# Kernel optimization log

Hardware: AMD Instinct MI355X
Metric: run time of the kernel (lower is better)

Reference implementation:

```python
import jax, jax.numpy as jnp
import numpy as np

N = 500_000      # total points
B = 64           # graphs in batch
D_IN = 64        # input feature dim (conv.in_tensor_reps.dim)
D_HID = 128      # EdgeConv MLP hidden
D_OUT = 128      # EdgeConv MLP out


def setup_inputs() -> dict:
    key = jax.random.key(0)
    k = jax.random.split(key, 8)
    x = jax.random.normal(k[0], (N, D_IN), jnp.float32)
    pos = jax.random.normal(k[1], (N, 3), jnp.float32)
    batch = jnp.sort(jax.random.randint(k[2], (N,), 0, B, dtype=jnp.int32))
    lframes = jax.random.normal(k[3], (N, 3, 3), jnp.float32)
    fan1 = 2 * D_IN + 3
    W1 = jax.random.normal(k[4], (fan1, D_HID), jnp.float32) / np.sqrt(fan1)
    b1 = jnp.zeros((D_HID,), jnp.float32)
    W2 = jax.random.normal(k[5], (D_HID, D_OUT), jnp.float32) / np.sqrt(D_HID)
    b2 = jnp.zeros((D_OUT,), jnp.float32)
    return {"x": x, "pos": pos, "batch": batch, "lframes": lframes,
            "W1": W1, "b1": b1, "W2": W2, "b2": b2}


def reference(x, pos, batch, lframes, W1, b1, W2, b2):
    n = pos.shape[0]
    # scatter-mean: center of mass per graph
    counts = jax.ops.segment_sum(jnp.ones((n,), pos.dtype), batch, num_segments=B)
    coms = jax.ops.segment_sum(pos, batch, num_segments=B) / jnp.maximum(counts, 1.0)[:, None]
    # distance of each point to its graph's COM
    dist = jnp.linalg.norm(pos - coms[batch], axis=-1)
    # scatter-min argmin per graph (first occurrence, like torch_scatter.scatter_min)
    min_d = jax.ops.segment_min(dist, batch, num_segments=B)
    node_ids = jnp.arange(n, dtype=jnp.int32)
    cand = jnp.where(dist <= min_d[batch], node_ids, n)
    idx = jnp.minimum(jax.ops.segment_min(cand, batch, num_segments=B), n - 1)  # [B]
    # gathers for the destination (center) nodes
    x_dst = x[idx]          # [B, D_IN]
    pos_dst = pos[idx]      # [B, 3]
    lframes_dst = lframes[idx]  # [B, 3, 3]
    # EdgeConv over edge_index = [arange(N) -> batch]:
    # message_e = MLP([x_dst_i, x_src_j - x_dst_i, pos_j - pos_i]), max-aggregated per graph
    xd = x_dst[batch]                      # [N, D_IN]
    feat = jnp.concatenate([xd, x - xd, pos - pos_dst[batch]], axis=-1)  # [N, 2*D_IN+3]
    h = jax.nn.relu(feat @ W1 + b1)        # [N, D_HID]
    msg = h @ W2 + b2                      # [N, D_OUT]
    out = jax.ops.segment_max(msg, batch, num_segments=B)  # [B, D_OUT]
    return out, pos_dst, batch[idx], lframes_dst
```

## Files before the change

### kernel.cpp

```cpp
#include <hip/hip_runtime.h>
#include <hip/hip_bf16.h>

#define NPTS 500000
#define NGR  64
#define TR   128
#define NT2  ((NPTS + TR - 1) / TR)
#define CHUNK 4
#define NBLK ((NT2 + CHUNK - 1) / CHUNK)

typedef __bf16 bf16x8 __attribute__((ext_vector_type(8)));
typedef float f32x4 __attribute__((ext_vector_type(4)));
typedef unsigned int u32x4 __attribute__((ext_vector_type(4)));

#define OFF_OUTACC 6144
#define OFF_CBIAS  38912
#define OFF_W1PT   71680
#define OFF_W1AT   73728
#define OFF_W2T    90112

__device__ __forceinline__ unsigned mapf(float f) {
    union { float f; unsigned u; } v; v.f = f;
    return ((int)v.u >= 0) ? (v.u | 0x80000000u) : ~v.u;
}

#define GLOAD_LDS16(g, l) __builtin_amdgcn_global_load_lds(                 \
    (__attribute__((address_space(1))) void*)(g),                           \
    (__attribute__((address_space(3))) void*)(l), 16, 0, 0)

__global__ __launch_bounds__(1024) void k_pre(
                      const float* __restrict__ pos,
                      const int* __restrict__ batch,
                      const float* __restrict__ x,
                      const float* __restrict__ W1,
                      const float* __restrict__ b1,
                      const float* __restrict__ W2,
                      const float* __restrict__ lfr,
                      unsigned short* __restrict__ W1aT,
                      unsigned short* __restrict__ W2T,
                      float* __restrict__ W1pT,
                      unsigned* __restrict__ outacc,
                      float* __restrict__ cbias,
                      float* __restrict__ outf) {
    __shared__ double sd[16][3];
    __shared__ unsigned long long sk[16];
    __shared__ double scom[3];
    __shared__ int sid;
    __shared__ float sposd[3];
    __shared__ float sp[4][128];
    __shared__ int sse[2];

    int g = blockIdx.x, t = threadIdx.x;
    int lane = t & 63, wv = t >> 6;

    {
        int i = g * 1024 + t;
        if (i < 8192) {
            outacc[i] = 0u;
            int n = i >> 6, k = i & 63;
            unsigned short v = (unsigned short)(__builtin_bit_cast(unsigned, (float)(__bf16)W1[(64 + k) * 128 + n]) >> 16);
            W1aT[i ^ ((n & 7) << 3)] = v;
        } else if (i < 8192 + 16384) {
            int j = i - 8192; int n = j >> 7, k = j & 127;
            unsigned short v = (unsigned short)(__builtin_bit_cast(unsigned, (float)(__bf16)W2[k * 128 + n]) >> 16);
            W2T[j ^ ((n & 7) << 3)] = v;
        } else if (i < 8192 + 16384 + 512) {
            int j = i - 24576; int n = j >> 2, q = j & 3;
            W1pT[j] = (q < 3) ? W1[(128 + q) * 128 + n] : 0.f;
        }
    }

    if (t < 2) {
        int target = g + t;
        int lo = 0, hi = NPTS;
        while (lo < hi) {
            int mid = (lo + hi) >> 1;
            if (batch[mid] < target) lo = mid + 1; else hi = mid;
        }
        sse[t] = lo;
    }
    __syncthreads();
    int s = sse[0], e = sse[1];

    double sx = 0.0, sy = 0.0, sz = 0.0;
    for (int i = s + t; i < e; i += 1024) {
        sx += (double)pos[i * 3 + 0];
        sy += (double)pos[i * 3 + 1];
        sz += (double)pos[i * 3 + 2];
    }
    #pragma unroll
    for (int m = 1; m < 64; m <<= 1) {
        sx += __shfl_xor(sx, m);
        sy += __shfl_xor(sy, m);
        sz += __shfl_xor(sz, m);
    }
    if (lane == 0) { sd[wv][0] = sx; sd[wv][1] = sy; sd[wv][2] = sz; }
    __syncthreads();
    if (t == 0) {
        double ax = 0.0, ay = 0.0, az = 0.0;
        for (int q = 0; q < 16; ++q) { ax += sd[q][0]; ay += sd[q][1]; az += sd[q][2]; }
        double cnt = (double)(e - s);
        double rc = 1.0 / (cnt > 1.0 ? cnt : 1.0);
        scom[0] = ax * rc; scom[1] = ay * rc; scom[2] = az * rc;
    }
    __syncthreads();
    double cx = scom[0], cy = scom[1], cz = scom[2];

    unsigned long long key = ~0ULL;
    for (int i = s + t; i < e; i += 1024) {
        double dx = (double)pos[i * 3 + 0] - cx;
        double dy = (double)pos[i * 3 + 1] - cy;
        double dz = (double)pos[i * 3 + 2] - cz;
        double d2 = __builtin_fma(dx, dx, __builtin_fma(dy, dy, dz * dz));
        unsigned long long b = __builtin_bit_cast(unsigned long long, d2);
        unsigned long long k2 = (b & ~0xFFFFFULL) | (unsigned long long)i;
        key = k2 < key ? k2 : key;
    }
    #pragma unroll
    for (int m = 1; m < 64; m <<= 1) {
        unsigned long long o = __shfl_xor(key, m);
        key = o < key ? o : key;
    }
    if (lane == 0) sk[wv] = key;
    __syncthreads();
    if (t == 0) {
        unsigned long long k = sk[0];
        for (int q = 1; q < 16; ++q) if (sk[q] < k) k = sk[q];
        int id = (int)(k & 0xFFFFFULL);
        if (id > NPTS - 1) id = NPTS - 1;
        sid = id;
    }
    __syncthreads();
    int id = sid;

    if (t < 3) {
        float p = pos[id * 3 + t];
        sposd[t] = p;
        outf[8192 + g * 3 + t] = p;
    }
    if (t == 4) outf[8192 + 192 + g] = (float)batch[id];
    if (t < 9) outf[8192 + 256 + g * 9 + t] = lfr[id * 9 + t];

    if (t < 512) {
        int c = t & 127, p = t >> 7;
        float part = 0.f;
        #pragma unroll
        for (int kq = 0; kq < 16; ++kq) {
            int k = p * 16 + kq;
            float xd = x[id * 64 + k];
            part += xd * (W1[k * 128 + c] - W1[(64 + k) * 128 + c]);
        }
        sp[p][c] = part;
    }
    __syncthreads();
    if (t < 128) {
        int c = t;
        float sv = b1[c] + sp[0][c] + sp[1][c] + sp[2][c] + sp[3][c];
        sv -= sposd[0] * W1[128 * 128 + c] + sposd[1] * W1[129 * 128 + c] + sposd[2] * W1[130 * 128 + c];
        cbias[g * 128 + c] = sv;
    }
}

__global__ __launch_bounds__(512, 2) void k_main(
    const float* __restrict__ x,
    const float* __restrict__ pos,
    const int* __restrict__ batch,
    const unsigned short* __restrict__ W1aT,
    const unsigned short* __restrict__ W2T,
    const float* __restrict__ W1pT,
    const float* __restrict__ cbias,
    unsigned* __restrict__ outacc)
{
    __shared__ alignas(16) unsigned char smem[81920];

    const int tid  = threadIdx.x;
    const int w    = tid >> 6;
    const int lane = tid & 63;
    const int quad = lane >> 4;
    const int mr   = lane & 15;

    #pragma unroll
    for (int i = 0; i < 6; ++i)
        GLOAD_LDS16((const char*)W1aT + (i * 512 + tid) * 16,
                    (char*)smem + (i * 512 + tid) * 16);

    bf16x8 bfrE[8];
    #pragma unroll
    for (int t8 = 0; t8 < 8; ++t8) {
        f32x4 wp = *(const f32x4*)(W1pT + (t8 * 16 + mr) * 4);
        bf16x8 e = (bf16x8){0, 0, 0, 0, 0, 0, 0, 0};
        if (quad == 0) { e[0] = (__bf16)wp[0]; e[1] = (__bf16)wp[1]; e[2] = (__bf16)wp[2]; }
        bfrE[t8] = e;
    }

    __syncthreads();

    const unsigned short* sW1 = (const unsigned short*)smem;
    const unsigned short* sW2 = (const unsigned short*)(smem + 16384);
    __bf16* hsb = (__bf16*)(smem + 49152) + w * 2048;
    const unsigned short* hss = (const unsigned short*)hsb;

    const int tb = blockIdx.x * CHUNK;
    int te = tb + CHUNK; if (te > NT2) te = NT2;

    f32x4 av0, av1, av2, av3;
    float pv0, pv1, pv2;
    {
        int gr = tb * TR + 16 * w + mr; if (gr > NPTS - 1) gr = NPTS - 1;
        const float* xp = x + (size_t)gr * 64 + quad * 8;
        av0 = *(const f32x4*)(xp);
        av1 = *(const f32x4*)(xp + 4);
        av2 = *(const f32x4*)(xp + 32);
        av3 = *(const f32x4*)(xp + 36);
        pv0 = pos[gr * 3 + 0];
        pv1 = pos[gr * 3 + 1];
        pv2 = pos[gr * 3 + 2];
    }

    for (int t = tb; t < te; ++t) {
        const int row0 = t * TR + 16 * w;

        bf16x8 afr0, afr1;
        afr0[0] = (__bf16)av0[0]; afr0[1] = (__bf16)av0[1]; afr0[2] = (__bf16)av0[2]; afr0[3] = (__bf16)av0[3];
        afr0[4] = (__bf16)av1[0]; afr0[5] = (__bf16)av1[1]; afr0[6] = (__bf16)av1[2]; afr0[7] = (__bf16)av1[3];
        afr1[0] = (__bf16)av2[0]; afr1[1] = (__bf16)av2[1]; afr1[2] = (__bf16)av2[2]; afr1[3] = (__bf16)av2[3];
        afr1[4] = (__bf16)av3[0]; afr1[5] = (__bf16)av3[1]; afr1[6] = (__bf16)av3[2]; afr1[7] = (__bf16)av3[3];
        bf16x8 aE = (bf16x8){0, 0, 0, 0, 0, 0, 0, 0};
        if (quad == 0) {
            aE[0] = (__bf16)pv0; aE[1] = (__bf16)pv1; aE[2] = (__bf16)pv2;
        }

        if (t + 1 < te) {
            int gr = (t + 1) * TR + 16 * w + mr; if (gr > NPTS - 1) gr = NPTS - 1;
            const float* xp = x + (size_t)gr * 64 + quad * 8;
            av0 = *(const f32x4*)(xp);
            av1 = *(const f32x4*)(xp + 4);
            av2 = *(const f32x4*)(xp + 32);
            av3 = *(const f32x4*)(xp + 36);
            pv0 = pos[gr * 3 + 0];
            pv1 = pos[gr * 3 + 1];
            pv2 = pos[gr * 3 + 2];
        }

        int rowg[4]; bool rowv[4];
        #pragma unroll
        for (int r = 0; r < 4; ++r) {
            int gr = row0 + quad * 4 + r;
            rowv[r] = (gr < NPTS);
            rowg[r] = batch[gr < NPTS ? gr : NPTS - 1];
        }
        int gf = batch[row0 < NPTS ? row0 : NPTS - 1];
        int rl = row0 + 15; if (rl > NPTS - 1) rl = NPTS - 1;
        int gl = batch[rl];
        float cb0[8];
        #pragma unroll
        for (int t8 = 0; t8 < 8; ++t8) cb0[t8] = cbias[gf * 128 + t8 * 16 + mr];

        f32x4 acc[8];
        #pragma unroll
        for (int t8 = 0; t8 < 8; ++t8) acc[t8] = (f32x4){0.f, 0.f, 0.f, 0.f};
        #pragma unroll
        for (int t8 = 0; t8 < 8; ++t8) {
            int n = t8 * 16 + mr;
            int sw = (n & 7) << 3;
            bf16x8 bv0 = __builtin_bit_cast(bf16x8, *(const u32x4*)(sW1 + ((n * 64 + quad * 8) ^ sw)));
            bf16x8 bv1 = __builtin_bit_cast(bf16x8, *(const u32x4*)(sW1 + ((n * 64 + 32 + quad * 8) ^ sw)));
            acc[t8] = __builtin_amdgcn_mfma_f32_16x16x32_bf16(afr0, bv0, acc[t8], 0, 0, 0);
            acc[t8] = __builtin_amdgcn_mfma_f32_16x16x32_bf16(afr1, bv1, acc[t8], 0, 0, 0);
            acc[t8] = __builtin_amdgcn_mfma_f32_16x16x32_bf16(aE, bfrE[t8], acc[t8], 0, 0, 0);
        }

        #pragma unroll
        for (int r = 0; r < 4; ++r) {
            int lrow = quad * 4 + r;
            int g = rowg[r];
            bool odd = (g != gf);
            int sw = (lrow & 7) << 3;
            #pragma unroll
            for (int t8 = 0; t8 < 8; ++t8) {
                float cbv = cb0[t8];
                if (odd) cbv = cbias[g * 128 + t8 * 16 + mr];
                float v = fmaxf(acc[t8][r] + cbv, 0.f);
                hsb[lrow * 128 + ((t8 * 16 + mr) ^ sw)] = (__bf16)v;
            }
        }

        f32x4 acc2[8];
        #pragma unroll
        for (int t8 = 0; t8 < 8; ++t8) acc2[t8] = (f32x4){0.f, 0.f, 0.f, 0.f};
        int swr = (mr & 7) << 3;
        #pragma unroll
        for (int kk = 0; kk < 4; ++kk) {
            bf16x8 a2 = __builtin_bit_cast(bf16x8,
                *(const u32x4*)(hss + mr * 128 + ((kk * 32 + quad * 8) ^ swr)));
            #pragma unroll
            for (int t8 = 0; t8 < 8; ++t8) {
                int n = t8 * 16 + mr;
                bf16x8 bv = __builtin_bit_cast(bf16x8,
                    *(const u32x4*)(sW2 + ((n * 128 + kk * 32 + quad * 8) ^ ((n & 7) << 3))));
                acc2[t8] = __builtin_amdgcn_mfma_f32_16x16x32_bf16(a2, bv, acc2[t8], 0, 0, 0);
            }
        }

        for (int g = gf; g <= gl; ++g) {
            #pragma unroll
            for (int t8 = 0; t8 < 8; ++t8) {
                float m = -INFINITY;
                #pragma unroll
                for (int r = 0; r < 4; ++r)
                    if (rowv[r] && rowg[r] == g) m = fmaxf(m, acc2[t8][r]);
                m = fmaxf(m, __shfl_xor(m, 16));
                m = fmaxf(m, __shfl_xor(m, 32));
                unsigned mb = __builtin_bit_cast(unsigned, m);
                if (quad == 0 && mb != 0xFF800000u)
                    atomicMax(&outacc[g * 128 + t8 * 16 + mr], mapf(m));
            }
        }
    }
}

__global__ void k_out(const unsigned* __restrict__ outacc,
                      const float* __restrict__ b2v,
                      float* __restrict__ outf) {
    int i = blockIdx.x * 256 + threadIdx.x;
    unsigned key = outacc[i];
    float v;
    if (key == 0u) {
        v = -300.f;
    } else {
        unsigned bits = (key & 0x80000000u) ? (key & 0x7FFFFFFFu) : ~key;
        union { unsigned u; float f; } c; c.u = bits; v = c.f;
    }
    outf[i] = v + b2v[i & 127];
}

extern "C" void kernel_launch(void* const* d_in, const int* in_sizes, int n_in,
                              void* d_out, int out_size, void* d_ws, size_t ws_size,
                              hipStream_t stream) {
    const float* x   = (const float*)d_in[0];
    const float* pos = (const float*)d_in[1];
    const int*   bat = (const int*)d_in[2];
    const float* lfr = (const float*)d_in[3];
    const float* W1  = (const float*)d_in[4];
    const float* b1  = (const float*)d_in[5];
    const float* W2  = (const float*)d_in[6];
    const float* b2v = (const float*)d_in[7];
    float* outf = (float*)d_out;

    char* ws = (char*)d_ws;
    unsigned*       outacc = (unsigned*)(ws + OFF_OUTACC);
    float*          cbias  = (float*)(ws + OFF_CBIAS);
    float*          W1pT   = (float*)(ws + OFF_W1PT);
    unsigned short* W1aT   = (unsigned short*)(ws + OFF_W1AT);
    unsigned short* W2T    = (unsigned short*)(ws + OFF_W2T);

    k_pre<<<64, 1024, 0, stream>>>(pos, bat, x, W1, b1, W2, lfr,
                                   W1aT, W2T, W1pT, outacc, cbias, outf);
    k_main<<<NBLK, 512, 0, stream>>>(x, pos, bat, W1aT, W2T, W1pT, cbias, outacc);
    k_out<<<32, 256, 0, stream>>>(outacc, b2v, outf);
}
```

Before: 275.6 us.

## Add single-graph fast path, prefetch batch ids, and double chunk size

Prefetches the first and last graph ids of the next tile and caches the per-graph bias across iterations, reloading it only when the graph changes. Adds a fast path for tiles whose 16 rows all belong to one graph, which skips per-row batch loads, per-row bias selection and the per-graph masked max loop. Doubles CHUNK, so each block handles twice as many tiles and fewer blocks are launched. The larger chunk lowers the block count, which may reduce occupancy or cause load imbalance, and the branching adds some code size.

After: 256.9 us. 1.07x faster.

```diff
diff --git a/kernel.cpp b/kernel.cpp
--- a/kernel.cpp
+++ b/kernel.cpp
@@ -5,7 +5,7 @@
 #define NGR  64
 #define TR   128
 #define NT2  ((NPTS + TR - 1) / TR)
-#define CHUNK 4
+#define CHUNK 8
 #define NBLK ((NT2 + CHUNK - 1) / CHUNK)
 
 typedef __bf16 bf16x8 __attribute__((ext_vector_type(8)));
@@ -204,6 +204,7 @@
 
     f32x4 av0, av1, av2, av3;
     float pv0, pv1, pv2;
+    int gf, gl;
     {
         int gr = tb * TR + 16 * w + mr; if (gr > NPTS - 1) gr = NPTS - 1;
         const float* xp = x + (size_t)gr * 64 + quad * 8;
@@ -214,7 +215,14 @@
         pv0 = pos[gr * 3 + 0];
         pv1 = pos[gr * 3 + 1];
         pv2 = pos[gr * 3 + 2];
-    }
+        int r0 = tb * TR + 16 * w;
+        gf = batch[r0 < NPTS ? r0 : NPTS - 1];
+        int rl = r0 + 15; if (rl > NPTS - 1) rl = NPTS - 1;
+        gl = batch[rl];
+    }
+    float cb0[8];
+    #pragma unroll
+    for (int t8 = 0; t8 < 8; ++t8) cb0[t8] = cbias[gf * 128 + t8 * 16 + mr];
 
     for (int t = tb; t < te; ++t) {
         const int row0 = t * TR + 16 * w;
@@ -229,6 +237,7 @@
             aE[0] = (__bf16)pv0; aE[1] = (__bf16)pv1; aE[2] = (__bf16)pv2;
         }
 
+        int gfn = gf, gln = gl;
         if (t + 1 < te) {
             int gr = (t + 1) * TR + 16 * w + mr; if (gr > NPTS - 1) gr = NPTS - 1;
             const float* xp = x + (size_t)gr * 64 + quad * 8;
@@ -239,21 +248,11 @@
             pv0 = pos[gr * 3 + 0];
             pv1 = pos[gr * 3 + 1];
             pv2 = pos[gr * 3 + 2];
-        }
-
-        int rowg[4]; bool rowv[4];
-        #pragma unroll
-        for (int r = 0; r < 4; ++r) {
-            int gr = row0 + quad * 4 + r;
-            rowv[r] = (gr < NPTS);
-            rowg[r] = batch[gr < NPTS ? gr : NPTS - 1];
-        }
-        int gf = batch[row0 < NPTS ? row0 : NPTS - 1];
-        int rl = row0 + 15; if (rl > NPTS - 1) rl = NPTS - 1;
-        int gl = batch[rl];
-        float cb0[8];
-        #pragma unroll
-        for (int t8 = 0; t8 < 8; ++t8) cb0[t8] = cbias[gf * 128 + t8 * 16 + mr];
+            int r0n = (t + 1) * TR + 16 * w;
+            gfn = batch[r0n < NPTS ? r0n : NPTS - 1];
+            int rln = r0n + 15; if (rln > NPTS - 1) rln = NPTS - 1;
+            gln = batch[rln];
+        }
 
         f32x4 acc[8];
         #pragma unroll
@@ -269,18 +268,39 @@
             acc[t8] = __builtin_amdgcn_mfma_f32_16x16x32_bf16(aE, bfrE[t8], acc[t8], 0, 0, 0);
         }
 
-        #pragma unroll
-        for (int r = 0; r < 4; ++r) {
-            int lrow = quad * 4 + r;
-            int g = rowg[r];
-            bool odd = (g != gf);
-            int sw = (lrow & 7) << 3;
+        const bool fast = (gf == gl) && (row0 + 15 < NPTS);
+        int rowg[4]; bool rowv[4];
+        if (fast) {
             #pragma unroll
-            for (int t8 = 0; t8 < 8; ++t8) {
-                float cbv = cb0[t8];
-                if (odd) cbv = cbias[g * 128 + t8 * 16 + mr];
-                float v = fmaxf(acc[t8][r] + cbv, 0.f);
-                hsb[lrow * 128 + ((t8 * 16 + mr) ^ sw)] = (__bf16)v;
+            for (int r = 0; r < 4; ++r) {
+                int lrow = quad * 4 + r;
+                int sw = (lrow & 7) << 3;
+                #pragma unroll
+                for (int t8 = 0; t8 < 8; ++t8) {
+                    float v = fmaxf(acc[t8][r] + cb0[t8], 0.f);
+                    hsb[lrow * 128 + ((t8 * 16 + mr) ^ sw)] = (__bf16)v;
+                }
+            }
+        } else {
+            #pragma unroll
+            for (int r = 0; r < 4; ++r) {
+                int gr = row0 + quad * 4 + r;
+                rowv[r] = (gr < NPTS);
+                rowg[r] = batch[gr < NPTS ? gr : NPTS - 1];
+            }
+            #pragma unroll
+            for (int r = 0; r < 4; ++r) {
+                int lrow = quad * 4 + r;
+                int g = rowg[r];
+                bool odd = (g != gf);
+                int sw = (lrow & 7) << 3;
+                #pragma unroll
+                for (int t8 = 0; t8 < 8; ++t8) {
+                    float cbv = cb0[t8];
+                    if (odd) cbv = cbias[g * 128 + t8 * 16 + mr];
+                    float v = fmaxf(acc[t8][r] + cbv, 0.f);
+                    hsb[lrow * 128 + ((t8 * 16 + mr) ^ sw)] = (__bf16)v;
+                }
             }
         }
 
@@ -301,19 +321,39 @@
             }
         }
 
-        for (int g = gf; g <= gl; ++g) {
+        if (fast) {
             #pragma unroll
             for (int t8 = 0; t8 < 8; ++t8) {
-                float m = -INFINITY;
-                #pragma unroll
-                for (int r = 0; r < 4; ++r)
-                    if (rowv[r] && rowg[r] == g) m = fmaxf(m, acc2[t8][r]);
+                float m = fmaxf(fmaxf(acc2[t8][0], acc2[t8][1]),
+                                fmaxf(acc2[t8][2], acc2[t8][3]));
                 m = fmaxf(m, __shfl_xor(m, 16));
                 m = fmaxf(m, __shfl_xor(m, 32));
-                unsigned mb = __builtin_bit_cast(unsigned, m);
-                if (quad == 0 && mb != 0xFF800000u)
-                    atomicMax(&outacc[g * 128 + t8 * 16 + mr], mapf(m));
-            }
+                if (quad == 0)
+                    atomicMax(&outacc[gf * 128 + t8 * 16 + mr], mapf(m));
+            }
+        } else {
+            for (int g = gf; g <= gl; ++g) {
+                #pragma unroll
+                for (int t8 = 0; t8 < 8; ++t8) {
+                    float m = -INFINITY;
+                    #pragma unroll
+                    for (int r = 0; r < 4; ++r)
+                        if (rowv[r] && rowg[r] == g) m = fmaxf(m, acc2[t8][r]);
+                    m = fmaxf(m, __shfl_xor(m, 16));
+                    m = fmaxf(m, __shfl_xor(m, 32));
+                    unsigned mb = __builtin_bit_cast(unsigned, m);
+                    if (quad == 0 && mb != 0xFF800000u)
+                        atomicMax(&outacc[g * 128 + t8 * 16 + mr], mapf(m));
+                }
+            }
+        }
+
+        if (t + 1 < te) {
+            if (gfn != gf) {
+                #pragma unroll
+                for (int t8 = 0; t8 < 8; ++t8) cb0[t8] = cbias[gfn * 128 + t8 * 16 + mr];
+            }
+            gf = gfn; gl = gln;
         }
     }
 }
```
